# Performance work log

Hardware: AMD Instinct MI355X
Metric: run time of the kernel (lower is better)

The kernel has to match this reference:

```python
import jax, jax.numpy as jnp
import numpy as np

N = 500_000   # total points
B = 8         # scenes / segments
C = 64        # embedding_dim (= internal_dim, downsample_rate=1)
H = 8         # num_heads


def setup_inputs() -> dict:
    key = jax.random.key(0)
    ks = jax.random.split(key, 12)
    s = 1.0 / np.sqrt(C)
    q = jax.random.normal(ks[0], (N, C), jnp.float32)
    k = jax.random.normal(ks[1], (B, C), jnp.float32)
    v = jax.random.normal(ks[2], (B, C), jnp.float32)
    batch = jnp.sort(jax.random.randint(ks[3], (N,), 0, B)).astype(jnp.int64)
    Wq = jax.random.normal(ks[4], (C, C), jnp.float32) * s
    bq = jnp.zeros((C,), jnp.float32)
    Wk = jax.random.normal(ks[5], (C, C), jnp.float32) * s
    bk = jnp.zeros((C,), jnp.float32)
    Wv = jax.random.normal(ks[6], (C, C), jnp.float32) * s
    bv = jnp.zeros((C,), jnp.float32)
    Wo = jax.random.normal(ks[7], (C, C), jnp.float32) * s
    bo = jnp.zeros((C,), jnp.float32)
    return dict(q=q, k=k, v=v, Wq=Wq, bq=bq, Wk=Wk, bk=bk, Wv=Wv, bv=bv,
                Wo=Wo, bo=bo, batch=batch)


def reference(q, k, v, Wq, bq, Wk, bk, Wv, bv, Wo, bo, batch):
    # Linear projections (nn.Linear applies x @ W.T + b)
    qp = q @ Wq.T + bq            # [N, C]
    kp = k @ Wk.T + bk            # [B, C]
    vp = v @ Wv.T + bv            # [B, C]
    n, c = qp.shape
    d = c // H                    # c_per_head
    nb = kp.shape[0]
    qh = qp.reshape(n, H, d)
    kh = kp.reshape(nb, H, d)[batch]   # gather per point -> [N, H, d]
    vh = vp.reshape(nb, H, d)[batch]   # [N, H, d]
    # elementwise scores, scaled
    attn = qh * kh * (1.0 / np.sqrt(d))  # [N, H, d]
    # segment softmax over the point dim within each batch segment
    m = jax.ops.segment_max(attn, batch, num_segments=nb)   # [B, H, d]
    e = jnp.exp(attn - m[batch])
    z = jax.ops.segment_sum(e, batch, num_segments=nb)      # [B, H, d]
    a = e / z[batch]
    out = (a * vh).reshape(n, c)
    return out @ Wo.T + bo
```

## Files before the change

kernel.cpp:

```cpp
#include <hip/hip_runtime.h>
#include <math.h>

#define NPTS 500000
#define SCALE 0.35355339059327373f
#define NT128 3907
#define TPB 2
#define GRID ((NT128 + TPB - 1) / TPB)
#define Q4TOT 8000000

#define QTIDX(k, p) ((((k) >> 2) * 532) + (((k) & 3) * 132) + (p))
#define QT_SZ 8512


__global__ void prep_kernel(const float* __restrict__ kin, const float* __restrict__ vin,
                            const float* __restrict__ Wq, const float* __restrict__ Wk,
                            const float* __restrict__ bk, const float* __restrict__ Wv,
                            const float* __restrict__ bv, const float* __restrict__ Wo,
                            float* __restrict__ ws) {
    const int gid = blockIdx.x * 256 + threadIdx.x;
    float* WqT = ws;
    float* WoT = ws + 4096;
    float* khs = ws + 8192;
    float* vh  = ws + 8704;
    double* zg = (double*)(ws + 9216);
    for (int idx = gid; idx < 4096; idx += 8 * 256) {
        int a = idx >> 6, b = idx & 63;
        WqT[idx] = Wq[b * 64 + a];
        WoT[idx] = Wo[b * 64 + a];
    }
    for (int idx = gid; idx < 512; idx += 8 * 256) {
        int b = idx >> 6, c = idx & 63;
        float dk = 0.f, dv = 0.f;
        #pragma unroll 8
        for (int j = 0; j < 64; ++j) {
            dk = fmaf(kin[b * 64 + j], Wk[c * 64 + j], dk);
            dv = fmaf(vin[b * 64 + j], Wv[c * 64 + j], dv);
        }
        khs[idx] = (dk + bk[c]) * SCALE;
        vh[idx]  = dv + bv[c];
        zg[idx]  = 0.0;
    }
}


__global__ __launch_bounds__(256, 3) void passA_kernel(const float* __restrict__ q,
                                                       const int* __restrict__ batch,
                                                       const float* __restrict__ bq,
                                                       float* __restrict__ ws,
                                                       float* __restrict__ e_out) {
    __shared__ __align__(16) float qT[QT_SZ];
    __shared__ __align__(16) float wq[4096];
    __shared__ __align__(16) float khs_l[512];
    __shared__ __align__(16) float zred[256];

    const float* WqT   = ws;
    const float* khs_g = ws + 8192;
    double* zg = (double*)(ws + 9216);

    const int tid  = threadIdx.x;
    const int wid  = tid >> 6;
    const int lane = tid & 63;
    const int cc   = tid & 7;
    const int ty   = tid >> 3;

    for (int idx = tid; idx < 1024; idx += 256) ((float4*)wq)[idx] = ((const float4*)WqT)[idx];
    for (int idx = tid; idx < 128; idx += 256) ((float4*)khs_l)[idx] = ((const float4*)khs_g)[idx];

    float bqlo[4], bqhi[4];
    { float4 b4 = ((const float4*)bq)[cc];
      bqlo[0] = b4.x; bqlo[1] = b4.y; bqlo[2] = b4.z; bqlo[3] = b4.w;
      b4 = ((const float4*)bq)[8 + cc];
      bqhi[0] = b4.x; bqhi[1] = b4.y; bqhi[2] = b4.z; bqhi[3] = b4.w; }

    float zacc[8] = {};
    int cur_b = -1;

    auto flushz = [&](int b) {
        if (b < 0) return;
        #pragma unroll
        for (int j = 0; j < 8; ++j) {
            zacc[j] += __shfl_xor(zacc[j], 8);
            zacc[j] += __shfl_xor(zacc[j], 16);
            zacc[j] += __shfl_xor(zacc[j], 32);
        }
        __syncthreads();
        if ((lane >> 3) == 0) {
            *(float4*)&zred[wid * 64 + 4 * cc]      = make_float4(zacc[0], zacc[1], zacc[2], zacc[3]);
            *(float4*)&zred[wid * 64 + 32 + 4 * cc] = make_float4(zacc[4], zacc[5], zacc[6], zacc[7]);
        }
        __syncthreads();
        if (tid < 64) {
            float s = zred[tid] + zred[64 + tid] + zred[128 + tid] + zred[192 + tid];
            unsafeAtomicAdd(&zg[b * 64 + tid], (double)s);
        }
        #pragma unroll
        for (int j = 0; j < 8; ++j) zacc[j] = 0.f;
    };

    const int t0 = blockIdx.x * TPB;
    const int t1 = (t0 + TPB < NT128) ? (t0 + TPB) : NT128;
    __syncthreads();

    for (int t = t0; t < t1; ++t) {
        const int p0g = t * 128;

        #pragma unroll
        for (int i = 0; i < 8; ++i) {
            const int g4 = t * 2048 + i * 256 + tid;
            float4 v = make_float4(0.f, 0.f, 0.f, 0.f);
            if (g4 < Q4TOT) v = ((const float4*)q)[g4];
            const int pl = i * 16 + (tid >> 4);
            const int kc = tid & 15;
            qT[QTIDX(4 * kc + 0, pl)] = v.x;
            qT[QTIDX(4 * kc + 1, pl)] = v.y;
            qT[QTIDX(4 * kc + 2, pl)] = v.z;
            qT[QTIDX(4 * kc + 3, pl)] = v.w;
        }
        const int b_lo = batch[p0g];
        const int b_hi = batch[(p0g + 127 < NPTS) ? (p0g + 127) : (NPTS - 1)];
        const bool uni = (b_lo == b_hi);
        __syncthreads();

        if (uni) {
            if (cur_b != b_lo) { flushz(cur_b); cur_b = b_lo; }
        } else {
            flushz(cur_b);
            cur_b = -1;
        }

        float acc[4][8] = {};
        #pragma unroll 4
        for (int kc = 0; kc < 16; ++kc) {
            #pragma unroll
            for (int j = 0; j < 4; ++j) {
                const float4 a4  = *(const float4*)&qT[kc * 532 + j * 132 + 4 * ty];
                const float4 wlo = *(const float4*)&wq[(kc * 4 + j) * 64 + 4 * cc];
                const float4 whi = *(const float4*)&wq[(kc * 4 + j) * 64 + 32 + 4 * cc];
                const float av[4] = {a4.x, a4.y, a4.z, a4.w};
                const float wl[4] = {wlo.x, wlo.y, wlo.z, wlo.w};
                const float wh[4] = {whi.x, whi.y, whi.z, whi.w};
                #pragma unroll
                for (int i = 0; i < 4; ++i) {
                    #pragma unroll
                    for (int m = 0; m < 4; ++m) {
                        acc[i][m]     = fmaf(av[i], wl[m], acc[i][m]);
                        acc[i][4 + m] = fmaf(av[i], wh[m], acc[i][4 + m]);
                    }
                }
            }
        }

        if (uni) {
            const float4 klo = *(const float4*)&khs_l[b_lo * 64 + 4 * cc];
            const float4 khi = *(const float4*)&khs_l[b_lo * 64 + 32 + 4 * cc];
            const float kl[4] = {klo.x, klo.y, klo.z, klo.w};
            const float kh[4] = {khi.x, khi.y, khi.z, khi.w};
            #pragma unroll
            for (int i = 0; i < 4; ++i) {
                const int gp = p0g + 4 * ty + i;
                if (gp < NPTS) {
                    float e0[4], e1[4];
                    #pragma unroll
                    for (int m = 0; m < 4; ++m) {
                        e0[m] = __expf((acc[i][m] + bqlo[m]) * kl[m]);
                        e1[m] = __expf((acc[i][4 + m] + bqhi[m]) * kh[m]);
                    }
                    ((float4*)e_out)[gp * 16 + cc]     = make_float4(e0[0], e0[1], e0[2], e0[3]);
                    ((float4*)e_out)[gp * 16 + 8 + cc] = make_float4(e1[0], e1[1], e1[2], e1[3]);
                    #pragma unroll
                    for (int m = 0; m < 4; ++m) { zacc[m] += e0[m]; zacc[4 + m] += e1[m]; }
                }
            }
        } else {
            #pragma unroll
            for (int i = 0; i < 4; ++i) {
                const int gp = p0g + 4 * ty + i;
                if (gp < NPTS) {
                    const int bi = batch[gp];
                    const float4 klo = *(const float4*)&khs_l[bi * 64 + 4 * cc];
                    const float4 khi = *(const float4*)&khs_l[bi * 64 + 32 + 4 * cc];
                    const float kl[4] = {klo.x, klo.y, klo.z, klo.w};
                    const float kh[4] = {khi.x, khi.y, khi.z, khi.w};
                    float e0[4], e1[4];
                    #pragma unroll
                    for (int m = 0; m < 4; ++m) {
                        e0[m] = __expf((acc[i][m] + bqlo[m]) * kl[m]);
                        e1[m] = __expf((acc[i][4 + m] + bqhi[m]) * kh[m]);
                    }
                    ((float4*)e_out)[gp * 16 + cc]     = make_float4(e0[0], e0[1], e0[2], e0[3]);
                    ((float4*)e_out)[gp * 16 + 8 + cc] = make_float4(e1[0], e1[1], e1[2], e1[3]);
                    #pragma unroll
                    for (int m = 0; m < 4; ++m) {
                        unsafeAtomicAdd(&zg[bi * 64 + 4 * cc + m], (double)e0[m]);
                        unsafeAtomicAdd(&zg[bi * 64 + 32 + 4 * cc + m], (double)e1[m]);
                    }
                }
            }
        }
        __syncthreads();
    }
    flushz(cur_b);
}

__global__ __launch_bounds__(256, 3) void passB_kernel(const int* __restrict__ batch,
                                                       const float* __restrict__ bo,
                                                       const float* __restrict__ ws,
                                                       float* __restrict__ out) {
    __shared__ __align__(16) float tT[QT_SZ];
    __shared__ __align__(16) float wo[4096];
    __shared__ __align__(16) float w_l[512];

    const float* WoT  = ws + 4096;
    const float* vh_g = ws + 8704;
    const double* zg  = (const double*)(ws + 9216);

    const int tid = threadIdx.x;
    const int cc  = tid & 7;
    const int ty  = tid >> 3;

    for (int idx = tid; idx < 1024; idx += 256) ((float4*)wo)[idx] = ((const float4*)WoT)[idx];
    for (int idx = tid; idx < 512; idx += 256)
        w_l[idx] = (float)((double)vh_g[idx] / zg[idx]);

    float bolo[4], bohi[4];
    { float4 b4 = ((const float4*)bo)[cc];
      bolo[0] = b4.x; bolo[1] = b4.y; bolo[2] = b4.z; bolo[3] = b4.w;
      b4 = ((const float4*)bo)[8 + cc];
      bohi[0] = b4.x; bohi[1] = b4.y; bohi[2] = b4.z; bohi[3] = b4.w; }

    const int t0 = blockIdx.x * TPB;
    const int t1 = (t0 + TPB < NT128) ? (t0 + TPB) : NT128;
    __syncthreads();

    for (int t = t0; t < t1; ++t) {
        const int p0g = t * 128;
        const int b_lo = batch[p0g];
        const int b_hi = batch[(p0g + 127 < NPTS) ? (p0g + 127) : (NPTS - 1)];
        const bool uni = (b_lo == b_hi);

        #pragma unroll
        for (int i = 0; i < 8; ++i) {
            const int g4 = t * 2048 + i * 256 + tid;
            float4 v = make_float4(0.f, 0.f, 0.f, 0.f);
            if (g4 < Q4TOT) v = ((const float4*)out)[g4];
            const int pl = i * 16 + (tid >> 4);
            const int kc = tid & 15;
            int bi = b_lo;
            if (!uni) {
                const int gp = p0g + pl;
                bi = batch[(gp < NPTS) ? gp : (NPTS - 1)];
            }
            const float4 wv = *(const float4*)&w_l[bi * 64 + 4 * kc];
            tT[QTIDX(4 * kc + 0, pl)] = v.x * wv.x;
            tT[QTIDX(4 * kc + 1, pl)] = v.y * wv.y;
            tT[QTIDX(4 * kc + 2, pl)] = v.z * wv.z;
            tT[QTIDX(4 * kc + 3, pl)] = v.w * wv.w;
        }
        __syncthreads();

        float acc[4][8] = {};
        #pragma unroll 4
        for (int kc = 0; kc < 16; ++kc) {
            #pragma unroll
            for (int j = 0; j < 4; ++j) {
                const float4 a4  = *(const float4*)&tT[kc * 532 + j * 132 + 4 * ty];
                const float4 wlo = *(const float4*)&wo[(kc * 4 + j) * 64 + 4 * cc];
                const float4 whi = *(const float4*)&wo[(kc * 4 + j) * 64 + 32 + 4 * cc];
                const float av[4] = {a4.x, a4.y, a4.z, a4.w};
                const float wl[4] = {wlo.x, wlo.y, wlo.z, wlo.w};
                const float wh[4] = {whi.x, whi.y, whi.z, whi.w};
                #pragma unroll
                for (int i = 0; i < 4; ++i) {
                    #pragma unroll
                    for (int m = 0; m < 4; ++m) {
                        acc[i][m]     = fmaf(av[i], wl[m], acc[i][m]);
                        acc[i][4 + m] = fmaf(av[i], wh[m], acc[i][4 + m]);
                    }
                }
            }
        }

        #pragma unroll
        for (int i = 0; i < 4; ++i) {
            const int gp = p0g + 4 * ty + i;
            if (gp < NPTS) {
                ((float4*)out)[gp * 16 + cc] =
                    make_float4(acc[i][0] + bolo[0], acc[i][1] + bolo[1],
                                acc[i][2] + bolo[2], acc[i][3] + bolo[3]);
                ((float4*)out)[gp * 16 + 8 + cc] =
                    make_float4(acc[i][4] + bohi[0], acc[i][5] + bohi[1],
                                acc[i][6] + bohi[2], acc[i][7] + bohi[3]);
            }
        }
        __syncthreads();
    }
}

extern "C" void kernel_launch(void* const* d_in, const int* in_sizes, int n_in,
                              void* d_out, int out_size, void* d_ws, size_t ws_size,
                              hipStream_t stream) {
    const float* q   = (const float*)d_in[0];
    const float* k   = (const float*)d_in[1];
    const float* v   = (const float*)d_in[2];
    const float* Wq  = (const float*)d_in[3];
    const float* bq  = (const float*)d_in[4];
    const float* Wk  = (const float*)d_in[5];
    const float* bk  = (const float*)d_in[6];
    const float* Wv  = (const float*)d_in[7];
    const float* bv  = (const float*)d_in[8];
    const float* Wo  = (const float*)d_in[9];
    const float* bo  = (const float*)d_in[10];
    const int*  batch = (const int*)d_in[11];
    float* out = (float*)d_out;
    float* ws  = (float*)d_ws;

    prep_kernel<<<8, 256, 0, stream>>>(k, v, Wq, Wk, bk, Wv, bv, Wo, ws);
    passA_kernel<<<GRID, 256, 0, stream>>>(q, batch, bq, ws, out);
    passB_kernel<<<GRID, 256, 0, stream>>>(batch, bo, ws, out);
}
```

Before: 349.6 us.

## Stage tiles via async global-to-LDS loads with swizzled layout and 8x8 register tiles

Replaces the manual transposed LDS staging of q and out tiles with global_load_lds direct copies into an XOR-swizzled row layout. Each thread now computes an 8x8 output tile from float4 dot-product reads, and blocks shrink to 128 threads handling 4 tiles each. In pass B the per-segment softmax weight is folded into Wo when a tile has a single segment, so activations are only rescaled on mixed tiles. The weight transposes move out of the prep kernel into each block. This adds register pressure and changes LDS bank patterns, and the async loads appear to lack explicit waits before the barrier.

```diff
diff --git a/kernel.cpp b/kernel.cpp
--- a/kernel.cpp
+++ b/kernel.cpp
@@ -1,33 +1,46 @@
 #include <hip/hip_runtime.h>
 #include <math.h>
+#include <stdint.h>
 
 #define NPTS 500000
 #define SCALE 0.35355339059327373f
 #define NT128 3907
-#define TPB 2
+#define TPB 4
 #define GRID ((NT128 + TPB - 1) / TPB)
 #define Q4TOT 8000000
 
-#define QTIDX(k, p) ((((k) >> 2) * 532) + (((k) & 3) * 132) + (p))
-#define QT_SZ 8512
-
+
+
+__device__ __forceinline__ void gload_lds16(const float* g, float* l) {
+    __builtin_amdgcn_global_load_lds(
+        (const __attribute__((address_space(1))) void*)g,
+        (__attribute__((address_space(3))) void*)l, 16, 0, 0);
+}
+
+__device__ __forceinline__ void stage_tile_async(const float* __restrict__ gsrc,
+                                                 int t, float* lds, int tid) {
+    const int wv   = tid >> 6;
+    const int ln   = tid & 63;
+    const int lrow = ln >> 4;
+    const int j    = ln & 15;
+    #pragma unroll
+    for (int qi = 0; qi < 16; ++qi) {
+        const int chunk = wv * 16 + qi;
+        const int row   = chunk * 4 + lrow;
+        int g4 = t * 2048 + row * 16 + (j ^ ((row >> 3) & 7));
+        if (g4 >= Q4TOT) g4 = 0;
+        gload_lds16(gsrc + (size_t)g4 * 4, lds + chunk * 256);
+    }
+}
 
 __global__ void prep_kernel(const float* __restrict__ kin, const float* __restrict__ vin,
-                            const float* __restrict__ Wq, const float* __restrict__ Wk,
-                            const float* __restrict__ bk, const float* __restrict__ Wv,
-                            const float* __restrict__ bv, const float* __restrict__ Wo,
+                            const float* __restrict__ Wk, const float* __restrict__ bk,
+                            const float* __restrict__ Wv, const float* __restrict__ bv,
                             float* __restrict__ ws) {
     const int gid = blockIdx.x * 256 + threadIdx.x;
-    float* WqT = ws;
-    float* WoT = ws + 4096;
     float* khs = ws + 8192;
     float* vh  = ws + 8704;
     double* zg = (double*)(ws + 9216);
-    for (int idx = gid; idx < 4096; idx += 8 * 256) {
-        int a = idx >> 6, b = idx & 63;
-        WqT[idx] = Wq[b * 64 + a];
-        WoT[idx] = Wo[b * 64 + a];
-    }
     for (int idx = gid; idx < 512; idx += 8 * 256) {
         int b = idx >> 6, c = idx & 63;
         float dk = 0.f, dv = 0.f;
@@ -43,34 +56,71 @@
 }
 
 
-__global__ __launch_bounds__(256, 3) void passA_kernel(const float* __restrict__ q,
+#define GEMM88(TILE4, W4)                                                    \
+    _Pragma("unroll 4")                                                      \
+    for (int kq = 0; kq < 16; ++kq) {                                        \
+        float4 av[8], wv[8];                                                 \
+        _Pragma("unroll")                                                    \
+        for (int i = 0; i < 8; ++i) av[i] = (TILE4)[ab[i] ^ kq];             \
+        _Pragma("unroll")                                                    \
+        for (int m = 0; m < 8; ++m) wv[m] = (W4)[wb[m] ^ kq];                \
+        _Pragma("unroll")                                                    \
+        for (int i = 0; i < 8; ++i) {                                        \
+            _Pragma("unroll")                                                \
+            for (int m = 0; m < 8; ++m) {                                    \
+                acc[i][m] = fmaf(av[i].x, wv[m].x, acc[i][m]);               \
+                acc[i][m] = fmaf(av[i].y, wv[m].y, acc[i][m]);               \
+                acc[i][m] = fmaf(av[i].z, wv[m].z, acc[i][m]);               \
+                acc[i][m] = fmaf(av[i].w, wv[m].w, acc[i][m]);               \
+            }                                                                \
+        }                                                                    \
+    }
+
+#define SETUP_BASES()                                                        \
+    int ab[8], wb[8];                                                        \
+    {                                                                        \
+        const int tyx = ty & 7;                                              \
+        _Pragma("unroll")                                                    \
+        for (int i = 0; i < 8; ++i) ab[i] = ((8 * ty + i) * 16) | tyx;       \
+        _Pragma("unroll")                                                    \
+        for (int m = 0; m < 4; ++m) {                                        \
+            wb[m]     = ((4 * cc + m) * 16) | cc;                            \
+            wb[4 + m] = ((32 + 4 * cc + m) * 16) | cc;                       \
+        }                                                                    \
+    }
+
+__global__ __launch_bounds__(128, 2) void passA_kernel(const float* __restrict__ q,
                                                        const int* __restrict__ batch,
                                                        const float* __restrict__ bq,
+                                                       const float* __restrict__ Wq,
                                                        float* __restrict__ ws,
                                                        float* __restrict__ e_out) {
-    __shared__ __align__(16) float qT[QT_SZ];
+    __shared__ __align__(16) float qT[8192];
     __shared__ __align__(16) float wq[4096];
     __shared__ __align__(16) float khs_l[512];
-    __shared__ __align__(16) float zred[256];
-
-    const float* WqT   = ws;
+    __shared__ __align__(16) float zred[128];
+
     const float* khs_g = ws + 8192;
     double* zg = (double*)(ws + 9216);
 
-    const int tid  = threadIdx.x;
-    const int wid  = tid >> 6;
-    const int lane = tid & 63;
-    const int cc   = tid & 7;
-    const int ty   = tid >> 3;
-
-    for (int idx = tid; idx < 1024; idx += 256) ((float4*)wq)[idx] = ((const float4*)WqT)[idx];
-    for (int idx = tid; idx < 128; idx += 256) ((float4*)khs_l)[idx] = ((const float4*)khs_g)[idx];
-
-    float bqlo[4], bqhi[4];
-    { float4 b4 = ((const float4*)bq)[cc];
-      bqlo[0] = b4.x; bqlo[1] = b4.y; bqlo[2] = b4.z; bqlo[3] = b4.w;
-      b4 = ((const float4*)bq)[8 + cc];
-      bqhi[0] = b4.x; bqhi[1] = b4.y; bqhi[2] = b4.z; bqhi[3] = b4.w; }
+    const int tid = threadIdx.x;
+    const int cc  = tid & 7;
+    const int ty  = tid >> 3;
+
+    const float4* qT4 = (const float4*)qT;
+    const float4* wq4c = (const float4*)wq;
+    float4* wq4 = (float4*)wq;
+
+    for (int idx = tid; idx < 1024; idx += 128) {
+        const int c = idx >> 4, sc = idx & 15;
+        const int kq = sc ^ ((c >> 2) & 7);
+        wq4[idx] = ((const float4*)Wq)[c * 16 + kq];
+    }
+    for (int idx = tid; idx < 128; idx += 128)
+        ((float4*)khs_l)[idx] = ((const float4*)khs_g)[idx];
+
+    const float4 bqlo = ((const float4*)bq)[cc];
+    const float4 bqhi = ((const float4*)bq)[8 + cc];
 
     float zacc[8] = {};
     int cur_b = -1;
@@ -78,44 +128,36 @@
     auto flushz = [&](int b) {
         if (b < 0) return;
         #pragma unroll
-        for (int j = 0; j < 8; ++j) {
-            zacc[j] += __shfl_xor(zacc[j], 8);
-            zacc[j] += __shfl_xor(zacc[j], 16);
-            zacc[j] += __shfl_xor(zacc[j], 32);
-        }
-        __syncthreads();
-        if ((lane >> 3) == 0) {
-            *(float4*)&zred[wid * 64 + 4 * cc]      = make_float4(zacc[0], zacc[1], zacc[2], zacc[3]);
-            *(float4*)&zred[wid * 64 + 32 + 4 * cc] = make_float4(zacc[4], zacc[5], zacc[6], zacc[7]);
+        for (int jj = 0; jj < 8; ++jj) {
+            zacc[jj] += __shfl_xor(zacc[jj], 8);
+            zacc[jj] += __shfl_xor(zacc[jj], 16);
+            zacc[jj] += __shfl_xor(zacc[jj], 32);
+        }
+        __syncthreads();
+        if ((tid & 56) == 0) {
+            const int wv = tid >> 6;
+            *(float4*)&zred[wv * 64 + 4 * cc] =
+                make_float4(zacc[0], zacc[1], zacc[2], zacc[3]);
+            *(float4*)&zred[wv * 64 + 32 + 4 * cc] =
+                make_float4(zacc[4], zacc[5], zacc[6], zacc[7]);
         }
         __syncthreads();
         if (tid < 64) {
-            float s = zred[tid] + zred[64 + tid] + zred[128 + tid] + zred[192 + tid];
+            float s = zred[tid] + zred[64 + tid];
             unsafeAtomicAdd(&zg[b * 64 + tid], (double)s);
         }
         #pragma unroll
-        for (int j = 0; j < 8; ++j) zacc[j] = 0.f;
+        for (int jj = 0; jj < 8; ++jj) zacc[jj] = 0.f;
     };
 
     const int t0 = blockIdx.x * TPB;
     const int t1 = (t0 + TPB < NT128) ? (t0 + TPB) : NT128;
-    __syncthreads();
+
+    SETUP_BASES();
 
     for (int t = t0; t < t1; ++t) {
         const int p0g = t * 128;
-
-        #pragma unroll
-        for (int i = 0; i < 8; ++i) {
-            const int g4 = t * 2048 + i * 256 + tid;
-            float4 v = make_float4(0.f, 0.f, 0.f, 0.f);
-            if (g4 < Q4TOT) v = ((const float4*)q)[g4];
-            const int pl = i * 16 + (tid >> 4);
-            const int kc = tid & 15;
-            qT[QTIDX(4 * kc + 0, pl)] = v.x;
-            qT[QTIDX(4 * kc + 1, pl)] = v.y;
-            qT[QTIDX(4 * kc + 2, pl)] = v.z;
-            qT[QTIDX(4 * kc + 3, pl)] = v.w;
-        }
+        stage_tile_async(q, t, qT, tid);
         const int b_lo = batch[p0g];
         const int b_hi = batch[(p0g + 127 < NPTS) ? (p0g + 127) : (NPTS - 1)];
         const bool uni = (b_lo == b_hi);
@@ -128,72 +170,59 @@
             cur_b = -1;
         }
 
-        float acc[4][8] = {};
-        #pragma unroll 4
-        for (int kc = 0; kc < 16; ++kc) {
-            #pragma unroll
-            for (int j = 0; j < 4; ++j) {
-                const float4 a4  = *(const float4*)&qT[kc * 532 + j * 132 + 4 * ty];
-                const float4 wlo = *(const float4*)&wq[(kc * 4 + j) * 64 + 4 * cc];
-                const float4 whi = *(const float4*)&wq[(kc * 4 + j) * 64 + 32 + 4 * cc];
-                const float av[4] = {a4.x, a4.y, a4.z, a4.w};
-                const float wl[4] = {wlo.x, wlo.y, wlo.z, wlo.w};
-                const float wh[4] = {whi.x, whi.y, whi.z, whi.w};
-                #pragma unroll
-                for (int i = 0; i < 4; ++i) {
-                    #pragma unroll
-                    for (int m = 0; m < 4; ++m) {
-                        acc[i][m]     = fmaf(av[i], wl[m], acc[i][m]);
-                        acc[i][4 + m] = fmaf(av[i], wh[m], acc[i][4 + m]);
-                    }
-                }
-            }
-        }
-
+        float acc[8][8] = {};
+        GEMM88(qT4, wq4c);
+
+        const int pbase = p0g + 8 * ty;
         if (uni) {
             const float4 klo = *(const float4*)&khs_l[b_lo * 64 + 4 * cc];
             const float4 khi = *(const float4*)&khs_l[b_lo * 64 + 32 + 4 * cc];
-            const float kl[4] = {klo.x, klo.y, klo.z, klo.w};
-            const float kh[4] = {khi.x, khi.y, khi.z, khi.w};
             #pragma unroll
-            for (int i = 0; i < 4; ++i) {
-                const int gp = p0g + 4 * ty + i;
+            for (int i = 0; i < 8; ++i) {
+                const int gp = pbase + i;
                 if (gp < NPTS) {
-                    float e0[4], e1[4];
-                    #pragma unroll
-                    for (int m = 0; m < 4; ++m) {
-                        e0[m] = __expf((acc[i][m] + bqlo[m]) * kl[m]);
-                        e1[m] = __expf((acc[i][4 + m] + bqhi[m]) * kh[m]);
-                    }
-                    ((float4*)e_out)[gp * 16 + cc]     = make_float4(e0[0], e0[1], e0[2], e0[3]);
-                    ((float4*)e_out)[gp * 16 + 8 + cc] = make_float4(e1[0], e1[1], e1[2], e1[3]);
-                    #pragma unroll
-                    for (int m = 0; m < 4; ++m) { zacc[m] += e0[m]; zacc[4 + m] += e1[m]; }
+                    float4 e0, e1;
+                    e0.x = __expf((acc[i][0] + bqlo.x) * klo.x);
+                    e0.y = __expf((acc[i][1] + bqlo.y) * klo.y);
+                    e0.z = __expf((acc[i][2] + bqlo.z) * klo.z);
+                    e0.w = __expf((acc[i][3] + bqlo.w) * klo.w);
+                    e1.x = __expf((acc[i][4] + bqhi.x) * khi.x);
+                    e1.y = __expf((acc[i][5] + bqhi.y) * khi.y);
+                    e1.z = __expf((acc[i][6] + bqhi.z) * khi.z);
+                    e1.w = __expf((acc[i][7] + bqhi.w) * khi.w);
+                    ((float4*)e_out)[gp * 16 + cc]     = e0;
+                    ((float4*)e_out)[gp * 16 + 8 + cc] = e1;
+                    zacc[0] += e0.x; zacc[1] += e0.y; zacc[2] += e0.z; zacc[3] += e0.w;
+                    zacc[4] += e1.x; zacc[5] += e1.y; zacc[6] += e1.z; zacc[7] += e1.w;
                 }
             }
         } else {
             #pragma unroll
-            for (int i = 0; i < 4; ++i) {
-                const int gp = p0g + 4 * ty + i;
+            for (int i = 0; i < 8; ++i) {
+                const int gp = pbase + i;
                 if (gp < NPTS) {
                     const int bi = batch[gp];
                     const float4 klo = *(const float4*)&khs_l[bi * 64 + 4 * cc];
                     const float4 khi = *(const float4*)&khs_l[bi * 64 + 32 + 4 * cc];
-                    const float kl[4] = {klo.x, klo.y, klo.z, klo.w};
-                    const float kh[4] = {khi.x, khi.y, khi.z, khi.w};
-                    float e0[4], e1[4];
-                    #pragma unroll
-                    for (int m = 0; m < 4; ++m) {
-                        e0[m] = __expf((acc[i][m] + bqlo[m]) * kl[m]);
-                        e1[m] = __expf((acc[i][4 + m] + bqhi[m]) * kh[m]);
-                    }
-                    ((float4*)e_out)[gp * 16 + cc]     = make_float4(e0[0], e0[1], e0[2], e0[3]);
-                    ((float4*)e_out)[gp * 16 + 8 + cc] = make_float4(e1[0], e1[1], e1[2], e1[3]);
-                    #pragma unroll
-                    for (int m = 0; m < 4; ++m) {
-                        unsafeAtomicAdd(&zg[bi * 64 + 4 * cc + m], (double)e0[m]);
-                        unsafeAtomicAdd(&zg[bi * 64 + 32 + 4 * cc + m], (double)e1[m]);
-                    }
+                    float4 e0, e1;
+                    e0.x = __expf((acc[i][0] + bqlo.x) * klo.x);
+                    e0.y = __expf((acc[i][1] + bqlo.y) * klo.y);
+                    e0.z = __expf((acc[i][2] + bqlo.z) * klo.z);
+                    e0.w = __expf((acc[i][3] + bqlo.w) * klo.w);
+                    e1.x = __expf((acc[i][4] + bqhi.x) * khi.x);
+                    e1.y = __expf((acc[i][5] + bqhi.y) * khi.y);
+                    e1.z = __expf((acc[i][6] + bqhi.z) * khi.z);
+                    e1.w = __expf((acc[i][7] + bqhi.w) * khi.w);
+                    ((float4*)e_out)[gp * 16 + cc]     = e0;
+                    ((float4*)e_out)[gp * 16 + 8 + cc] = e1;
+                    unsafeAtomicAdd(&zg[bi * 64 + 4 * cc + 0], (double)e0.x);
+                    unsafeAtomicAdd(&zg[bi * 64 + 4 * cc + 1], (double)e0.y);
+                    unsafeAtomicAdd(&zg[bi * 64 + 4 * cc + 2], (double)e0.z);
+                    unsafeAtomicAdd(&zg[bi * 64 + 4 * cc + 3], (double)e0.w);
+                    unsafeAtomicAdd(&zg[bi * 64 + 32 + 4 * cc + 0], (double)e1.x);
+                    unsafeAtomicAdd(&zg[bi * 64 + 32 + 4 * cc + 1], (double)e1.y);
+                    unsafeAtomicAdd(&zg[bi * 64 + 32 + 4 * cc + 2], (double)e1.z);
+                    unsafeAtomicAdd(&zg[bi * 64 + 32 + 4 * cc + 3], (double)e1.w);
                 }
             }
         }
@@ -202,15 +231,15 @@
     flushz(cur_b);
 }
 
-__global__ __launch_bounds__(256, 3) void passB_kernel(const int* __restrict__ batch,
+__global__ __launch_bounds__(128, 2) void passB_kernel(const int* __restrict__ batch,
                                                        const float* __restrict__ bo,
+                                                       const float* __restrict__ Wo,
                                                        const float* __restrict__ ws,
                                                        float* __restrict__ out) {
-    __shared__ __align__(16) float tT[QT_SZ];
-    __shared__ __align__(16) float wo[4096];
+    __shared__ __align__(16) float tT[8192];
+    __shared__ __align__(16) float wp[4096];
     __shared__ __align__(16) float w_l[512];
 
-    const float* WoT  = ws + 4096;
     const float* vh_g = ws + 8704;
     const double* zg  = (const double*)(ws + 9216);
 
@@ -218,78 +247,76 @@
     const int cc  = tid & 7;
     const int ty  = tid >> 3;
 
-    for (int idx = tid; idx < 1024; idx += 256) ((float4*)wo)[idx] = ((const float4*)WoT)[idx];
-    for (int idx = tid; idx < 512; idx += 256)
+    const float4* tT4c = (const float4*)tT;
+    float4* tT4 = (float4*)tT;
+    const float4* wp4c = (const float4*)wp;
+    float4* wp4 = (float4*)wp;
+
+    for (int idx = tid; idx < 512; idx += 128)
         w_l[idx] = (float)((double)vh_g[idx] / zg[idx]);
 
-    float bolo[4], bohi[4];
-    { float4 b4 = ((const float4*)bo)[cc];
-      bolo[0] = b4.x; bolo[1] = b4.y; bolo[2] = b4.z; bolo[3] = b4.w;
-      b4 = ((const float4*)bo)[8 + cc];
-      bohi[0] = b4.x; bohi[1] = b4.y; bohi[2] = b4.z; bohi[3] = b4.w; }
+    const float4 bolo = ((const float4*)bo)[cc];
+    const float4 bohi = ((const float4*)bo)[8 + cc];
+
+    auto stage_wp = [&](int b) {
+        for (int idx = tid; idx < 1024; idx += 128) {
+            const int c2 = idx >> 4, sc = idx & 15;
+            const int kq = sc ^ ((c2 >> 2) & 7);
+            float4 wv4 = ((const float4*)Wo)[c2 * 16 + kq];
+            if (b >= 0) {
+                const float4 f = *(const float4*)&w_l[b * 64 + 4 * kq];
+                wv4.x *= f.x; wv4.y *= f.y; wv4.z *= f.z; wv4.w *= f.w;
+            }
+            wp4[idx] = wv4;
+        }
+    };
 
     const int t0 = blockIdx.x * TPB;
     const int t1 = (t0 + TPB < NT128) ? (t0 + TPB) : NT128;
+
+    SETUP_BASES();
+
+    int wb_cur = -2;
     __syncthreads();
 
     for (int t = t0; t < t1; ++t) {
         const int p0g = t * 128;
+        stage_tile_async(out, t, tT, tid);
         const int b_lo = batch[p0g];
         const int b_hi = batch[(p0g + 127 < NPTS) ? (p0g + 127) : (NPTS - 1)];
         const bool uni = (b_lo == b_hi);
-
+        const int want = uni ? b_lo : -1;
+        if (want != wb_cur) { stage_wp(want); wb_cur = want; }
+        __syncthreads();
+
+        if (!uni) {
+            const int gp = p0g + tid;
+            const int bi = batch[(gp < NPTS) ? gp : (NPTS - 1)];
+            #pragma unroll
+            for (int sc = 0; sc < 16; ++sc) {
+                const int kq = sc ^ ((tid >> 3) & 7);
+                float4 t4 = tT4[tid * 16 + sc];
+                const float4 f = *(const float4*)&w_l[bi * 64 + 4 * kq];
+                t4.x *= f.x; t4.y *= f.y; t4.z *= f.z; t4.w *= f.w;
+                tT4[tid * 16 + sc] = t4;
+            }
+            __syncthreads();
+        }
+
+        float acc[8][8] = {};
+        GEMM88(tT4c, wp4c);
+
+        const int pbase = p0g + 8 * ty;
         #pragma unroll
         for (int i = 0; i < 8; ++i) {
-            const int g4 = t * 2048 + i * 256 + tid;
-            float4 v = make_float4(0.f, 0.f, 0.f, 0.f);
-            if (g4 < Q4TOT) v = ((const float4*)out)[g4];
-            const int pl = i * 16 + (tid >> 4);
-            const int kc = tid & 15;
-            int bi = b_lo;
-            if (!uni) {
-                const int gp = p0g + pl;
-                bi = batch[(gp < NPTS) ? gp : (NPTS - 1)];
-            }
-            const float4 wv = *(const float4*)&w_l[bi * 64 + 4 * kc];
-            tT[QTIDX(4 * kc + 0, pl)] = v.x * wv.x;
-            tT[QTIDX(4 * kc + 1, pl)] = v.y * wv.y;
-            tT[QTIDX(4 * kc + 2, pl)] = v.z * wv.z;
-            tT[QTIDX(4 * kc + 3, pl)] = v.w * wv.w;
-        }
-        __syncthreads();
-
-        float acc[4][8] = {};
-        #pragma unroll 4
-        for (int kc = 0; kc < 16; ++kc) {
-            #pragma unroll
-            for (int j = 0; j < 4; ++j) {
-                const float4 a4  = *(const float4*)&tT[kc * 532 + j * 132 + 4 * ty];
-                const float4 wlo = *(const float4*)&wo[(kc * 4 + j) * 64 + 4 * cc];
-                const float4 whi = *(const float4*)&wo[(kc * 4 + j) * 64 + 32 + 4 * cc];
-                const float av[4] = {a4.x, a4.y, a4.z, a4.w};
-                const float wl[4] = {wlo.x, wlo.y, wlo.z, wlo.w};
-                const float wh[4] = {whi.x, whi.y, whi.z, whi.w};
-                #pragma unroll
-                for (int i = 0; i < 4; ++i) {
-                    #pragma unroll
-                    for (int m = 0; m < 4; ++m) {
-                        acc[i][m]     = fmaf(av[i], wl[m], acc[i][m]);
-                        acc[i][4 + m] = fmaf(av[i], wh[m], acc[i][4 + m]);
-                    }
-                }
-            }
-        }
-
-        #pragma unroll
-        for (int i = 0; i < 4; ++i) {
-            const int gp = p0g + 4 * ty + i;
+            const int gp = pbase + i;
             if (gp < NPTS) {
                 ((float4*)out)[gp * 16 + cc] =
-                    make_float4(acc[i][0] + bolo[0], acc[i][1] + bolo[1],
-                                acc[i][2] + bolo[2], acc[i][3] + bolo[3]);
+                    make_float4(acc[i][0] + bolo.x, acc[i][1] + bolo.y,
+                                acc[i][2] + bolo.z, acc[i][3] + bolo.w);
                 ((float4*)out)[gp * 16 + 8 + cc] =
-                    make_float4(acc[i][4] + bohi[0], acc[i][5] + bohi[1],
-                                acc[i][6] + bohi[2], acc[i][7] + bohi[3]);
+                    make_float4(acc[i][4] + bohi.x, acc[i][5] + bohi.y,
+                                acc[i][6] + bohi.z, acc[i][7] + bohi.w);
             }
         }
         __syncthreads();
@@ -314,7 +341,7 @@
     float* out = (float*)d_out;
     float* ws  = (float*)d_ws;
 
-    prep_kernel<<<8, 256, 0, stream>>>(k, v, Wq, Wk, bk, Wv, bv, Wo, ws);
-    passA_kernel<<<GRID, 256, 0, stream>>>(q, batch, bq, ws, out);
-    passB_kernel<<<GRID, 256, 0, stream>>>(batch, bo, ws, out);
-}
+    prep_kernel<<<8, 256, 0, stream>>>(k, v, Wk, bk, Wv, bv, ws);
+    passA_kernel<<<GRID, 128, 0, stream>>>(q, batch, bq, Wq, ws, out);
+    passB_kernel<<<GRID, 128, 0, stream>>>(batch, bo, Wo, ws, out);
+}
```

Result: slower. 399.6 us (+14.3%).
